# Kernel optimization log

Hardware: AMD Instinct MI355X
Metric: run time of the kernel (lower is better)

Reference implementation:

```python
import jax, jax.numpy as jnp
import numpy as np

NUM_E = 1024        # codebook size
E_DIM = 256         # embedding dim (== channels of x)
BETA = 0.25

def setup_inputs() -> dict:
    key = jax.random.key(0)
    kx, kw = jax.random.split(key)
    x = jax.random.normal(kx, (16, E_DIM, 64, 64), dtype=jnp.float32)
    # embedding weight init: uniform(-1/num_e, 1/e_dim), matching torch init
    codebook = jax.random.uniform(kw, (NUM_E, E_DIM), dtype=jnp.float32,
                                  minval=-1.0 / NUM_E, maxval=1.0 / E_DIM)
    return {"x": x, "codebook": codebook}

def reference(x, codebook):
    beta = BETA
    # NCHW -> NHWC, flatten to [N, D]
    xp = jnp.transpose(x, (0, 2, 3, 1))          # [B,H,W,D]
    x_shape = xp.shape
    xf = xp.reshape(-1, E_DIM)                   # [N,D]
    cb_sq = jnp.sum(codebook ** 2, axis=1)                 # [K]
    in_sq = jnp.sum(xf ** 2, axis=1, keepdims=True)        # [N,1]
    dist = in_sq + cb_sq - 2.0 * (xf @ codebook.T)         # [N,K]
    idx = jnp.argmin(dist, axis=1)                         # [N]
    # one-hot encodings (returned like the torch module)
    encodings = jax.nn.one_hot(idx, NUM_E, dtype=jnp.float32)  # [N,K]
    # one-hot @ codebook == gather; use gather (same math, no big GEMM)
    xq = jnp.take(codebook, idx, axis=0).reshape(x_shape)      # [B,H,W,D]
    embedding_loss = jnp.mean((jax.lax.stop_gradient(xq) - xp) ** 2)
    quantization_loss = jnp.mean((xq - jax.lax.stop_gradient(xp)) ** 2)
    loss = quantization_loss + beta * embedding_loss
    e_mean = jnp.mean(encodings, axis=0)
    # NOTE: original code uses +1e10 inside the log (likely a typo for 1e-10);
    # we reproduce it faithfully.
    perplexity = jnp.exp(-jnp.sum(e_mean * jnp.log(e_mean + 10000000000.0)))
    # straight-through estimator
    xq_st = xp + jax.lax.stop_gradient(xq - xp)
    xq_out = jnp.transpose(xq_st, (0, 3, 1, 2))  # NHWC -> NCHW
    return (loss, xq_out, perplexity, encodings)
```

## Files before the change

kernel.cpp:

```cpp
#include <hip/hip_runtime.h>
#include <math.h>
#include <stdint.h>

typedef float f4u __attribute__((ext_vector_type(4), aligned(4)));
typedef unsigned int u4v __attribute__((ext_vector_type(4)));
typedef __attribute__((ext_vector_type(8))) short short8;
typedef __attribute__((ext_vector_type(4))) float float4v;

#define DIM 256
#define KCB 1024
#define PERP_OFF 16777217
#define ENC_OFF  16777218
#define CAP 32
#define EPS 0.008f
#define NPB 128
#define SCORE_BLOCKS 512

__device__ __forceinline__ float np_sumsq128(const float* a, int stride) {
  float r[8];
  #pragma unroll
  for (int j = 0; j < 8; ++j) { float v = a[j * stride]; r[j] = __fmul_rn(v, v); }
  #pragma unroll
  for (int i = 8; i < 128; i += 8) {
    #pragma unroll
    for (int j = 0; j < 8; ++j) {
      float v = a[(i + j) * stride];
      r[j] = __fadd_rn(r[j], __fmul_rn(v, v));
    }
  }
  float s01 = __fadd_rn(r[0], r[1]);
  float s23 = __fadd_rn(r[2], r[3]);
  float s45 = __fadd_rn(r[4], r[5]);
  float s67 = __fadd_rn(r[6], r[7]);
  return __fadd_rn(__fadd_rn(s01, s23), __fadd_rn(s45, s67));
}

__device__ __forceinline__ unsigned short f2bf(float f) {
  unsigned u = __float_as_uint(f);
  u += 0x7FFFu + ((u >> 16) & 1u);
  return (unsigned short)(u >> 16);
}

__global__ __launch_bounds__(64)
void k_prep(const float* __restrict__ cb, unsigned short* __restrict__ e_bf16,
            float* __restrict__ cb_sq, int* __restrict__ counts) {
  const int k = blockIdx.x;
  const int l = threadIdx.x;
  float4 v = ((const float4*)(cb + k * DIM))[l];
  unsigned short bs[4] = {f2bf(v.x), f2bf(v.y), f2bf(v.z), f2bf(v.w)};
  *(ushort4*)(e_bf16 + k * DIM + l * 4) = *(ushort4*)bs;
  if (l == 0) {
    const float* p = cb + k * DIM;
    cb_sq[k] = __fadd_rn(np_sumsq128(p, 1), np_sumsq128(p + 128, 1));
    counts[k] = 0;
  }
}

__global__ __launch_bounds__(256, 3)
void k_score(const float* __restrict__ x, const unsigned short* __restrict__ e_bf16,
             const float* __restrict__ cb_sq, unsigned int* __restrict__ gcnt,
             unsigned short* __restrict__ glist, float* __restrict__ in_sq) {
  if (blockIdx.x >= SCORE_BLOCKS) {
    const int n = (blockIdx.x - SCORE_BLOCKS) * 256 + threadIdx.x;
    const int b = n >> 12;
    const int hw = n & 4095;
    const float* p = x + b * 1048576 + hw;
    float h0 = np_sumsq128(p, 4096);
    float h1 = np_sumsq128(p + 128 * 4096, 4096);
    in_sq[n] = __fadd_rn(h0, h1);
    return;
  }

  __shared__ unsigned int   lcnt[NPB];
  __shared__ unsigned short llist[NPB * CAP];
  __shared__ float          lsc[NPB * CAP];
  __shared__ float          lmin[NPB];
  const int t    = threadIdx.x;
  const int wv   = t >> 6;
  const int lane = t & 63;
  const int l15  = lane & 15;
  const int quad = lane >> 4;
  if (t < NPB) lcnt[t] = 0;
  __syncthreads();

  short8 Bf[2][8];
  const int nbase = blockIdx.x * NPB + wv * 32;
  #pragma unroll
  for (int g = 0; g < 2; ++g) {
    const int n = nbase + g * 16 + l15;
    const float* xb = x + (n >> 12) * 1048576 + (n & 4095);
    #pragma unroll
    for (int ks = 0; ks < 8; ++ks) {
      const int d0 = ks * 32 + quad * 8;
      union { unsigned short s[8]; short8 v; } u;
      #pragma unroll
      for (int j = 0; j < 8; ++j) u.s[j] = f2bf(xb[(d0 + j) * 4096]);
      Bf[g][ks] = u.v;
    }
  }

  float m[2] = {1e30f, 1e30f};
  for (int ct = 0; ct < 64; ++ct) {
    float4v acc[2];
    #pragma unroll
    for (int g = 0; g < 2; ++g) acc[g] = (float4v){0.f, 0.f, 0.f, 0.f};
    const unsigned short* ap = e_bf16 + (ct * 16 + l15) * DIM + quad * 8;
    #pragma unroll
    for (int ks = 0; ks < 8; ++ks) {
      const short8 a = *(const short8*)(ap + ks * 32);
      #pragma unroll
      for (int g = 0; g < 2; ++g)
        acc[g] = __builtin_amdgcn_mfma_f32_16x16x32_bf16(a, Bf[g][ks], acc[g], 0, 0, 0);
    }
    const float4 cs = *(const float4*)(cb_sq + ct * 16 + quad * 4);
    #pragma unroll
    for (int g = 0; g < 2; ++g) {
      const float sa[4] = {fmaf(-2.f, acc[g].x, cs.x), fmaf(-2.f, acc[g].y, cs.y),
                           fmaf(-2.f, acc[g].z, cs.z), fmaf(-2.f, acc[g].w, cs.w)};
      float bm = fminf(fminf(sa[0], sa[1]), fminf(sa[2], sa[3]));
      bm = fminf(bm, m[g]);
      bm = fminf(bm, __shfl_xor(bm, 16));
      bm = fminf(bm, __shfl_xor(bm, 32));
      m[g] = bm;
      const float thr = bm + EPS;
      const float sblk = fminf(fminf(sa[0], sa[1]), fminf(sa[2], sa[3]));
      if (sblk <= thr) {
        const int nl = wv * 32 + g * 16 + l15;
        #pragma unroll
        for (int r = 0; r < 4; ++r) {
          if (sa[r] <= thr) {
            unsigned slot = atomicAdd(&lcnt[nl], 1u);
            if (slot < CAP) {
              llist[nl * CAP + slot] = (unsigned short)(ct * 16 + quad * 4 + r);
              lsc[nl * CAP + slot]   = sa[r];
            }
          }
        }
      }
    }
  }
  if (quad == 0) {
    #pragma unroll
    for (int g = 0; g < 2; ++g) lmin[wv * 32 + g * 16 + l15] = m[g];
  }
  __syncthreads();

  if (t < NPB) {
    const unsigned cnt = lcnt[t];
    unsigned outc = cnt;
    if (cnt <= CAP) {
      const float thrf = lmin[t] + EPS;
      unsigned j = 0;
      for (unsigned i = 0; i < cnt; ++i) {
        const unsigned short c = llist[t * CAP + i];
        if (lsc[t * CAP + i] <= thrf) llist[t * CAP + j++] = c;
      }
      outc = j;
    }
    gcnt[blockIdx.x * NPB + t] = outc;

    u4v* gdst = (u4v*)(glist + (size_t)blockIdx.x * NPB * CAP);
    const u4v* lsrc = (const u4v*)llist;
    #pragma unroll
    for (int j = 0; j < 4; ++j)
      __builtin_nontemporal_store(lsrc[t * 4 + j], gdst + t * 4 + j);
  }
}

__global__ __launch_bounds__(256)
void k_refine(const float* __restrict__ x, const float* __restrict__ cb,
              const float* __restrict__ cb_sq, const float* __restrict__ in_sq,
              const unsigned int* __restrict__ gcnt,
              const unsigned short* __restrict__ glist,
              int* __restrict__ best_idx) {
  const int tid  = blockIdx.x * 256 + threadIdx.x;
  const int n    = tid >> 1;
  const int half = tid & 1;
  const unsigned cnt = gcnt[n];
  const float* xb = x + (n >> 12) * 1048576 + (n & 4095);
  const float isq = in_sq[n];
  float bv = 1e30f; int bc = 0x7FFFFFFF;

  if (cnt <= CAP) {
    const unsigned short* lst = glist + (size_t)n * CAP;
    for (unsigned i = half; i < cnt; i += 4) {
      const int c1 = lst[i];
      const bool has2 = (i + 2) < cnt;
      const int c2 = has2 ? lst[i + 2] : c1;
      const float4* e1 = (const float4*)(cb + c1 * DIM);
      const float4* e2 = (const float4*)(cb + c2 * DIM);
      float d1 = 0.f, d2 = 0.f;
      #pragma unroll 4
      for (int q = 0; q < 64; ++q) {
        const float4 a  = e1[q];
        const float4 bq = e2[q];
        const float x0 = xb[(q * 4 + 0) * 4096];
        const float x1 = xb[(q * 4 + 1) * 4096];
        const float x2 = xb[(q * 4 + 2) * 4096];
        const float x3 = xb[(q * 4 + 3) * 4096];
        d1 = fmaf(x0, a.x, d1);   d2 = fmaf(x0, bq.x, d2);
        d1 = fmaf(x1, a.y, d1);   d2 = fmaf(x1, bq.y, d2);
        d1 = fmaf(x2, a.z, d1);   d2 = fmaf(x2, bq.z, d2);
        d1 = fmaf(x3, a.w, d1);   d2 = fmaf(x3, bq.w, d2);
      }
      {
        const float dist = __fsub_rn(__fadd_rn(isq, cb_sq[c1]), __fmul_rn(2.f, d1));
        if (dist < bv || (dist == bv && c1 < bc)) { bv = dist; bc = c1; }
      }
      if (has2) {
        const float dist = __fsub_rn(__fadd_rn(isq, cb_sq[c2]), __fmul_rn(2.f, d2));
        if (dist < bv || (dist == bv && c2 < bc)) { bv = dist; bc = c2; }
      }
    }
  } else {
    for (int c = half; c < KCB; c += 2) {
      const float4* e1 = (const float4*)(cb + c * DIM);
      float d1 = 0.f;
      #pragma unroll 4
      for (int q = 0; q < 64; ++q) {
        const float4 a = e1[q];
        d1 = fmaf(xb[(q * 4 + 0) * 4096], a.x, d1);
        d1 = fmaf(xb[(q * 4 + 1) * 4096], a.y, d1);
        d1 = fmaf(xb[(q * 4 + 2) * 4096], a.z, d1);
        d1 = fmaf(xb[(q * 4 + 3) * 4096], a.w, d1);
      }
      const float dist = __fsub_rn(__fadd_rn(isq, cb_sq[c]), __fmul_rn(2.f, d1));
      if (dist < bv || (dist == bv && c < bc)) { bv = dist; bc = c; }
    }
  }
  const float ov = __shfl_xor(bv, 1);
  const int   oc = __shfl_xor(bc, 1);
  if (ov < bv || (ov == bv && oc < bc)) { bv = ov; bc = oc; }
  if (half == 0) best_idx[n] = bc;
}

__global__ __launch_bounds__(256)
void k_epi(const float* __restrict__ x, const float* __restrict__ cb,
           const int* __restrict__ best_idx, float* __restrict__ out1,
           float* __restrict__ enc, int* __restrict__ counts,
           double* __restrict__ partials) {
  const int t  = threadIdx.x;
  const int bh = blockIdx.x;
  const int b  = bh >> 6, h = bh & 63;
  __shared__ int idxs[64];
  if (t < 64) {
    const int myidx = best_idx[bh * 64 + t];
    idxs[t] = myidx;
    atomicAdd(counts + myidx, 1);
  }
  __syncthreads();

  {
    float* base = enc + (size_t)bh * 65536 + t * 4;
    #pragma unroll 8
    for (int r = 0; r < 64; ++r) {
      const int bi = idxs[r];
      f4u v = {0.f, 0.f, 0.f, 0.f};
      if ((bi >> 2) == t) {
        if ((bi & 3) == 0) v.x = 1.f; else if ((bi & 3) == 1) v.y = 1.f;
        else if ((bi & 3) == 2) v.z = 1.f; else v.w = 1.f;
      }
      __builtin_nontemporal_store(v, (f4u*)(base + r * 1024));
    }
  }

  const int w4 = (t & 15) * 4;
  const int cg = t >> 4;
  float qf[4][16];
  #pragma unroll
  for (int i = 0; i < 4; ++i) {
    const float4* rp = (const float4*)(cb + idxs[w4 + i] * DIM + cg * 16);
    #pragma unroll
    for (int jq = 0; jq < 4; ++jq) {
      const float4 v = rp[jq];
      qf[i][jq * 4 + 0] = v.x; qf[i][jq * 4 + 1] = v.y;
      qf[i][jq * 4 + 2] = v.z; qf[i][jq * 4 + 3] = v.w;
    }
  }

  double s = 0.0;
  #pragma unroll
  for (int j = 0; j < 16; ++j) {
    const int c = cg * 16 + j;
    const size_t off = ((size_t)b << 20) + ((size_t)c << 12) + (h << 6) + w4;
    const float4 xp = *(const float4*)(x + off);
    const float q0 = qf[0][j], q1 = qf[1][j], q2 = qf[2][j], q3 = qf[3][j];
    const float d0 = __fsub_rn(q0, xp.x), d1 = __fsub_rn(q1, xp.y);
    const float d2 = __fsub_rn(q2, xp.z), d3 = __fsub_rn(q3, xp.w);
    f4u o;
    o.x = __fadd_rn(xp.x, d0); o.y = __fadd_rn(xp.y, d1);
    o.z = __fadd_rn(xp.z, d2); o.w = __fadd_rn(xp.w, d3);
    __builtin_nontemporal_store(o, (f4u*)(out1 + off));
    s += (double)(d0*d0) + (double)(d1*d1) + (double)(d2*d2) + (double)(d3*d3);
  }
  #pragma unroll
  for (int off = 32; off > 0; off >>= 1) s += __shfl_down(s, off);
  __shared__ double sm[4];
  if ((t & 63) == 0) sm[t >> 6] = s;
  __syncthreads();
  if (t == 0) partials[bh] = (sm[0] + sm[1]) + (sm[2] + sm[3]);
}

__global__ __launch_bounds__(256)
void k_final(const double* __restrict__ partials, const int* __restrict__ counts,
             float* __restrict__ out) {
  const int t = threadIdx.x;
  double s = 0.0;
  #pragma unroll
  for (int i = 0; i < 4; ++i) s += partials[t + i * 256];
  #pragma unroll
  for (int off = 32; off > 0; off >>= 1) s += __shfl_down(s, off);
  __shared__ double sm[4];
  __shared__ float smf[4];
  if ((t & 63) == 0) sm[t >> 6] = s;

  float ps = 0.f;
  #pragma unroll
  for (int i = 0; i < 4; ++i) {
    const float p = (float)counts[t + i * 256] * (1.0f / 65536.0f);
    ps += p * logf(1.0e10f + p);
  }
  #pragma unroll
  for (int off = 32; off > 0; off >>= 1) ps += __shfl_down(ps, off);
  if ((t & 63) == 0) smf[t >> 6] = ps;
  __syncthreads();
  if (t == 0) {
    const double tot = (sm[0] + sm[1]) + (sm[2] + sm[3]);
    const float mval = (float)(tot / 16777216.0);
    out[0] = mval + 0.25f * mval;
    out[PERP_OFF] = expf(-((smf[0] + smf[1]) + (smf[2] + smf[3])));
  }
}

extern "C" void kernel_launch(void* const* d_in, const int* in_sizes, int n_in,
                              void* d_out, int out_size, void* d_ws, size_t ws_size,
                              hipStream_t stream) {
  const float* x  = (const float*)d_in[0];
  const float* cb = (const float*)d_in[1];
  float* out = (float*)d_out;
  char*  ws  = (char*)d_ws;

  int*            counts   = (int*)(ws + 0);
  float*          cb_sq    = (float*)(ws + 4096);
  int*            best_idx = (int*)(ws + 8192);
  float*          in_sq    = (float*)(ws + 270336);
  double*         partials = (double*)(ws + 532480);
  unsigned short* e_bf16   = (unsigned short*)(ws + 1589248);
  unsigned int*   gcnt     = (unsigned int*)(ws + 2113536);
  unsigned short* glist    = (unsigned short*)(ws + 2375680);

  k_prep  <<<1024, 64, 0, stream>>>(cb, e_bf16, cb_sq, counts);
  k_score <<<SCORE_BLOCKS + 256, 256, 0, stream>>>(x, e_bf16, cb_sq, gcnt, glist, in_sq);
  k_refine<<<512, 256, 0, stream>>>(x, cb, cb_sq, in_sq, gcnt, glist, best_idx);
  k_epi   <<<1024, 256, 0, stream>>>(x, cb, best_idx, out + 1,
                                     out + ENC_OFF, counts, partials);
  k_final <<<1, 256, 0, stream>>>(partials, counts, out);
}
```

Baseline: 638.5 us.

## Fuse refine and input-norm computation into epilogue kernel, drop separate passes

Removes the in_sq blocks from the score kernel and the separate refine kernel. The epilogue kernel now computes the per-row input norms into shared memory, refines the candidate lists with 4 threads per row, and passes the best index straight into the one-hot, loss and count work. This cuts two kernel launches and the global round-trips for in_sq and best_idx. The cost is that the norm computation now sits on the critical path before refinement, and each thread handles one candidate at a time instead of two interleaved.

```diff
diff --git a/kernel.cpp b/kernel.cpp
--- a/kernel.cpp
+++ b/kernel.cpp
@@ -59,18 +59,7 @@
 __global__ __launch_bounds__(256, 3)
 void k_score(const float* __restrict__ x, const unsigned short* __restrict__ e_bf16,
              const float* __restrict__ cb_sq, unsigned int* __restrict__ gcnt,
-             unsigned short* __restrict__ glist, float* __restrict__ in_sq) {
-  if (blockIdx.x >= SCORE_BLOCKS) {
-    const int n = (blockIdx.x - SCORE_BLOCKS) * 256 + threadIdx.x;
-    const int b = n >> 12;
-    const int hw = n & 4095;
-    const float* p = x + b * 1048576 + hw;
-    float h0 = np_sumsq128(p, 4096);
-    float h1 = np_sumsq128(p + 128 * 4096, 4096);
-    in_sq[n] = __fadd_rn(h0, h1);
-    return;
-  }
-
+             unsigned short* __restrict__ glist) {
   __shared__ unsigned int   lcnt[NPB];
   __shared__ unsigned short llist[NPB * CAP];
   __shared__ float          lsc[NPB * CAP];
@@ -168,85 +157,76 @@
 }
 
 __global__ __launch_bounds__(256)
-void k_refine(const float* __restrict__ x, const float* __restrict__ cb,
-              const float* __restrict__ cb_sq, const float* __restrict__ in_sq,
-              const unsigned int* __restrict__ gcnt,
-              const unsigned short* __restrict__ glist,
-              int* __restrict__ best_idx) {
-  const int tid  = blockIdx.x * 256 + threadIdx.x;
-  const int n    = tid >> 1;
-  const int half = tid & 1;
-  const unsigned cnt = gcnt[n];
-  const float* xb = x + (n >> 12) * 1048576 + (n & 4095);
-  const float isq = in_sq[n];
-  float bv = 1e30f; int bc = 0x7FFFFFFF;
-
-  if (cnt <= CAP) {
-    const unsigned short* lst = glist + (size_t)n * CAP;
-    for (unsigned i = half; i < cnt; i += 4) {
-      const int c1 = lst[i];
-      const bool has2 = (i + 2) < cnt;
-      const int c2 = has2 ? lst[i + 2] : c1;
-      const float4* e1 = (const float4*)(cb + c1 * DIM);
-      const float4* e2 = (const float4*)(cb + c2 * DIM);
-      float d1 = 0.f, d2 = 0.f;
-      #pragma unroll 4
-      for (int q = 0; q < 64; ++q) {
-        const float4 a  = e1[q];
-        const float4 bq = e2[q];
-        const float x0 = xb[(q * 4 + 0) * 4096];
-        const float x1 = xb[(q * 4 + 1) * 4096];
-        const float x2 = xb[(q * 4 + 2) * 4096];
-        const float x3 = xb[(q * 4 + 3) * 4096];
-        d1 = fmaf(x0, a.x, d1);   d2 = fmaf(x0, bq.x, d2);
-        d1 = fmaf(x1, a.y, d1);   d2 = fmaf(x1, bq.y, d2);
-        d1 = fmaf(x2, a.z, d1);   d2 = fmaf(x2, bq.z, d2);
-        d1 = fmaf(x3, a.w, d1);   d2 = fmaf(x3, bq.w, d2);
-      }
-      {
-        const float dist = __fsub_rn(__fadd_rn(isq, cb_sq[c1]), __fmul_rn(2.f, d1));
-        if (dist < bv || (dist == bv && c1 < bc)) { bv = dist; bc = c1; }
-      }
-      if (has2) {
-        const float dist = __fsub_rn(__fadd_rn(isq, cb_sq[c2]), __fmul_rn(2.f, d2));
-        if (dist < bv || (dist == bv && c2 < bc)) { bv = dist; bc = c2; }
-      }
-    }
-  } else {
-    for (int c = half; c < KCB; c += 2) {
-      const float4* e1 = (const float4*)(cb + c * DIM);
-      float d1 = 0.f;
-      #pragma unroll 4
-      for (int q = 0; q < 64; ++q) {
-        const float4 a = e1[q];
-        d1 = fmaf(xb[(q * 4 + 0) * 4096], a.x, d1);
-        d1 = fmaf(xb[(q * 4 + 1) * 4096], a.y, d1);
-        d1 = fmaf(xb[(q * 4 + 2) * 4096], a.z, d1);
-        d1 = fmaf(xb[(q * 4 + 3) * 4096], a.w, d1);
-      }
-      const float dist = __fsub_rn(__fadd_rn(isq, cb_sq[c]), __fmul_rn(2.f, d1));
-      if (dist < bv || (dist == bv && c < bc)) { bv = dist; bc = c; }
-    }
-  }
-  const float ov = __shfl_xor(bv, 1);
-  const int   oc = __shfl_xor(bc, 1);
-  if (ov < bv || (ov == bv && oc < bc)) { bv = ov; bc = oc; }
-  if (half == 0) best_idx[n] = bc;
-}
-
-__global__ __launch_bounds__(256)
-void k_epi(const float* __restrict__ x, const float* __restrict__ cb,
-           const int* __restrict__ best_idx, float* __restrict__ out1,
-           float* __restrict__ enc, int* __restrict__ counts,
-           double* __restrict__ partials) {
+void k_fused(const float* __restrict__ x, const float* __restrict__ cb,
+             const float* __restrict__ cb_sq,
+             const unsigned int* __restrict__ gcnt,
+             const unsigned short* __restrict__ glist,
+             float* __restrict__ out1, float* __restrict__ enc,
+             int* __restrict__ counts, double* __restrict__ partials) {
   const int t  = threadIdx.x;
   const int bh = blockIdx.x;
   const int b  = bh >> 6, h = bh & 63;
-  __shared__ int idxs[64];
+  __shared__ float isq_s[64];
+  __shared__ int   idxs[64];
+
   if (t < 64) {
-    const int myidx = best_idx[bh * 64 + t];
-    idxs[t] = myidx;
-    atomicAdd(counts + myidx, 1);
+    const int n = bh * 64 + t;
+    const float* p = x + b * 1048576 + (n & 4095);
+    float h0 = np_sumsq128(p, 4096);
+    float h1 = np_sumsq128(p + 128 * 4096, 4096);
+    isq_s[t] = __fadd_rn(h0, h1);
+  }
+  __syncthreads();
+
+  {
+    const int nl = t >> 2;
+    const int q  = t & 3;
+    const int n  = bh * 64 + nl;
+    const unsigned cnt = gcnt[n];
+    const float* xb = x + b * 1048576 + (n & 4095);
+    const float isq = isq_s[nl];
+    float bv = 1e30f; int bc = 0x7FFFFFFF;
+
+    if (cnt <= CAP) {
+      const unsigned short* lst = glist + (size_t)n * CAP;
+      for (unsigned i = q; i < cnt; i += 4) {
+        const int c1 = lst[i];
+        const float4* e1 = (const float4*)(cb + c1 * DIM);
+        float d1 = 0.f;
+        #pragma unroll 4
+        for (int qq = 0; qq < 64; ++qq) {
+          const float4 a = e1[qq];
+          d1 = fmaf(xb[(qq * 4 + 0) * 4096], a.x, d1);
+          d1 = fmaf(xb[(qq * 4 + 1) * 4096], a.y, d1);
+          d1 = fmaf(xb[(qq * 4 + 2) * 4096], a.z, d1);
+          d1 = fmaf(xb[(qq * 4 + 3) * 4096], a.w, d1);
+        }
+        const float dist = __fsub_rn(__fadd_rn(isq, cb_sq[c1]), __fmul_rn(2.f, d1));
+        if (dist < bv || (dist == bv && c1 < bc)) { bv = dist; bc = c1; }
+      }
+    } else {
+      for (int c = q; c < KCB; c += 4) {
+        const float4* e1 = (const float4*)(cb + c * DIM);
+        float d1 = 0.f;
+        #pragma unroll 4
+        for (int qq = 0; qq < 64; ++qq) {
+          const float4 a = e1[qq];
+          d1 = fmaf(xb[(qq * 4 + 0) * 4096], a.x, d1);
+          d1 = fmaf(xb[(qq * 4 + 1) * 4096], a.y, d1);
+          d1 = fmaf(xb[(qq * 4 + 2) * 4096], a.z, d1);
+          d1 = fmaf(xb[(qq * 4 + 3) * 4096], a.w, d1);
+        }
+        const float dist = __fsub_rn(__fadd_rn(isq, cb_sq[c]), __fmul_rn(2.f, d1));
+        if (dist < bv || (dist == bv && c < bc)) { bv = dist; bc = c; }
+      }
+    }
+    {
+      float ov = __shfl_xor(bv, 1); int oc = __shfl_xor(bc, 1);
+      if (ov < bv || (ov == bv && oc < bc)) { bv = ov; bc = oc; }
+      ov = __shfl_xor(bv, 2); oc = __shfl_xor(bc, 2);
+      if (ov < bv || (ov == bv && oc < bc)) { bv = ov; bc = oc; }
+    }
+    if (q == 0) { idxs[nl] = bc; atomicAdd(counts + bc, 1); }
   }
   __syncthreads();
 
@@ -342,17 +322,14 @@
 
   int*            counts   = (int*)(ws + 0);
   float*          cb_sq    = (float*)(ws + 4096);
-  int*            best_idx = (int*)(ws + 8192);
-  float*          in_sq    = (float*)(ws + 270336);
   double*         partials = (double*)(ws + 532480);
   unsigned short* e_bf16   = (unsigned short*)(ws + 1589248);
   unsigned int*   gcnt     = (unsigned int*)(ws + 2113536);
   unsigned short* glist    = (unsigned short*)(ws + 2375680);
 
   k_prep  <<<1024, 64, 0, stream>>>(cb, e_bf16, cb_sq, counts);
-  k_score <<<SCORE_BLOCKS + 256, 256, 0, stream>>>(x, e_bf16, cb_sq, gcnt, glist, in_sq);
-  k_refine<<<512, 256, 0, stream>>>(x, cb, cb_sq, in_sq, gcnt, glist, best_idx);
-  k_epi   <<<1024, 256, 0, stream>>>(x, cb, best_idx, out + 1,
+  k_score <<<SCORE_BLOCKS, 256, 0, stream>>>(x, e_bf16, cb_sq, gcnt, glist);
+  k_fused <<<1024, 256, 0, stream>>>(x, cb, cb_sq, gcnt, glist, out + 1,
                                      out + ENC_OFF, counts, partials);
   k_final <<<1, 256, 0, stream>>>(partials, counts, out);
 }
```

New measurement: 597.1 us. 1.07x faster.
